# Performance work log

Measured on AMD Instinct MI355X. Metric: run time of the kernel, lower is better.

Reference implementation:

```python
import jax, jax.numpy as jnp
import numpy as np

NUM_S = 50000
NUM_A = 50000
D = 64
H = 128
E = 1000000


def setup_inputs() -> dict:
    key = jax.random.key(0)
    ks = jax.random.split(key, 6)
    scale = 1.0 / np.sqrt(2 * D)
    return {
        "embeddings_s": jax.random.normal(ks[0], (NUM_S, D), dtype=jnp.float32),
        "embeddings_a": jax.random.normal(ks[1], (NUM_A, D), dtype=jnp.float32),
        "edge_index_sa": jax.random.randint(ks[2], (2, E), 0, NUM_S, dtype=jnp.int64),
        "W1": jax.random.normal(ks[3], (2 * D, H), dtype=jnp.float32) * scale,
        "b1": jnp.zeros((H,), dtype=jnp.float32),
        "W2": jax.random.normal(ks[4], (H, 1), dtype=jnp.float32) * (1.0 / np.sqrt(H)),
        "b2": jnp.zeros((1,), dtype=jnp.float32),
        "log_temperature": jnp.zeros((), dtype=jnp.float32),  # log(1.0)
    }


def reference(embeddings_s, embeddings_a, edge_index_sa, W1, b1, W2, b2, log_temperature):
    s_idx = edge_index_sa[0]
    a_idx = edge_index_sa[1]
    es = embeddings_s[s_idx]            # [E, D] gather
    ea = embeddings_a[a_idx]            # [E, D] gather
    diff = es - ea
    edge_costs = jnp.sqrt(jnp.sum(diff * diff, axis=1))  # torch.norm(dim=1)
    cat = jnp.concatenate([es, ea], axis=1)              # [E, 2D]
    h = jax.nn.relu(cat @ W1 + b1)                        # [E, H]
    gate = jax.nn.sigmoid(h @ W2 + b2)[:, 0]             # [E]
    edge_costs = edge_costs * gate
    temperature = jnp.exp(log_temperature)
    vals = -edge_costs / temperature
    # scatter_softmax over edges grouped by source node
    seg_max = jax.ops.segment_max(vals, s_idx, num_segments=NUM_S)
    ex = jnp.exp(vals - seg_max[s_idx])
    seg_sum = jax.ops.segment_sum(ex, s_idx, num_segments=NUM_S)
    edge_weights = ex / seg_sum[s_idx]
    return (edge_weights, edge_costs)
```

## Files before the change

### kernel.cpp

```cpp
#include <hip/hip_runtime.h>
#include <hip/hip_fp16.h>

#define D_NODE 64
#define H_DIM  128
#define REC_H  192

struct Half8 { __half2 h[4]; };

typedef _Float16 h2v __attribute__((ext_vector_type(2)));
struct H2x4 { h2v h[4]; };

#if defined(__has_builtin)
#  if __has_builtin(__builtin_amdgcn_fdot2)
#    define HAVE_FDOT2 1
#  endif
#endif

__global__ void __launch_bounds__(256)
prep_kernel(const float* __restrict__ emb_s,
            const float* __restrict__ emb_a,
            const float* __restrict__ W1,
            const float* __restrict__ b1,
            __half* __restrict__ recS,
            __half* __restrict__ recA,
            float* __restrict__ segsum,
            int numS, int numA, int pS, int pA)
{
    const int tid = threadIdx.x;
    int b = blockIdx.x;

    if (b >= pS + pA) {
        const int i = (b - pS - pA) * 256 + tid;
        if (i < numS) segsum[i] = 0.0f;
        return;
    }

    const bool isS = (b < pS);
    const int pb = isS ? b : b - pS;
    const float* etab = isS ? emb_s : emb_a;
    __half* rec = isS ? recS : recA;
    const int rowsTot = isS ? numS : numA;
    const int rowBase = pb * 64;

    __shared__ __half eT[64 * D_NODE];

    {
        const float4* src4 = (const float4*)(etab + (size_t)rowBase * D_NODE);
#pragma unroll
        for (int it = 0; it < 2; ++it) {
            const int c = tid + it * 256;
            const int row = c >> 3;
            const int sub = c & 7;
            const bool ok = (rowBase + row < rowsTot);
            float4 a = make_float4(0.f, 0.f, 0.f, 0.f), d = a;
            if (ok) { a = src4[2 * c]; d = src4[2 * c + 1]; }
            Half8 o;
            o.h[0] = __floats2half2_rn(a.x, a.y);
            o.h[1] = __floats2half2_rn(a.z, a.w);
            o.h[2] = __floats2half2_rn(d.x, d.y);
            o.h[3] = __floats2half2_rn(d.z, d.w);
            ((Half8*)eT)[c] = o;
            if (ok)
                ((Half8*)(rec + (size_t)(rowBase + row) * REC_H))[sub] = o;
        }
    }

    const int col = tid & 127;
    const int rhalf = tid >> 7;
    const float* Wh = isS ? W1 : (W1 + D_NODE * H_DIM);
    h2v w2[32];
#pragma unroll
    for (int k = 0; k < 32; ++k) {
        w2[k][0] = (_Float16)Wh[(2 * k) * H_DIM + col];
        w2[k][1] = (_Float16)Wh[(2 * k + 1) * H_DIM + col];
    }
    const float bias = isS ? b1[col] : 0.0f;

    __syncthreads();

    for (int r0 = rhalf * 32; r0 < rhalf * 32 + 32; r0 += 4) {
        const H2x4* e0 = (const H2x4*)&eT[(r0 + 0) * D_NODE];
        const H2x4* e1 = (const H2x4*)&eT[(r0 + 1) * D_NODE];
        const H2x4* e2 = (const H2x4*)&eT[(r0 + 2) * D_NODE];
        const H2x4* e3 = (const H2x4*)&eT[(r0 + 3) * D_NODE];
        float a0 = bias, a1 = bias, a2 = bias, a3 = bias;
#pragma unroll
        for (int k8 = 0; k8 < D_NODE / 8; ++k8) {
            const H2x4 v0 = e0[k8];
            const H2x4 v1 = e1[k8];
            const H2x4 v2 = e2[k8];
            const H2x4 v3 = e3[k8];
#pragma unroll
            for (int j = 0; j < 4; ++j) {
                const h2v w = w2[4 * k8 + j];
#ifdef HAVE_FDOT2
                a0 = __builtin_amdgcn_fdot2(v0.h[j], w, a0, false);
                a1 = __builtin_amdgcn_fdot2(v1.h[j], w, a1, false);
                a2 = __builtin_amdgcn_fdot2(v2.h[j], w, a2, false);
                a3 = __builtin_amdgcn_fdot2(v3.h[j], w, a3, false);
#else
                const float wx = (float)w[0], wy = (float)w[1];
                a0 = fmaf((float)v0.h[j][0], wx, a0); a0 = fmaf((float)v0.h[j][1], wy, a0);
                a1 = fmaf((float)v1.h[j][0], wx, a1); a1 = fmaf((float)v1.h[j][1], wy, a1);
                a2 = fmaf((float)v2.h[j][0], wx, a2); a2 = fmaf((float)v2.h[j][1], wy, a2);
                a3 = fmaf((float)v3.h[j][0], wx, a3); a3 = fmaf((float)v3.h[j][1], wy, a3);
#endif
            }
        }
        const int row = rowBase + r0;
        if (row + 0 < rowsTot)
            rec[(size_t)(row + 0) * REC_H + D_NODE + col] = __float2half(a0);
        if (row + 1 < rowsTot)
            rec[(size_t)(row + 1) * REC_H + D_NODE + col] = __float2half(a1);
        if (row + 2 < rowsTot)
            rec[(size_t)(row + 2) * REC_H + D_NODE + col] = __float2half(a2);
        if (row + 3 < rowsTot)
            rec[(size_t)(row + 3) * REC_H + D_NODE + col] = __float2half(a3);
    }
}

__global__ void __launch_bounds__(256)
edge_main_kernel(const __half* __restrict__ recS,
                 const __half* __restrict__ recA,
                 const int* __restrict__ idx,
                 const float* __restrict__ W2,
                 const float* __restrict__ b2,
                 const float* __restrict__ logT,
                 float* __restrict__ out_costs,
                 float* __restrict__ segsum,
                 int E)
{
    const int gid = blockIdx.x * 256 + (int)threadIdx.x;
    const int p = gid >> 3;
    const int t = gid & 7;
    const int e0 = 2 * p;
    const int e1 = 2 * p + 1;
    if (e0 >= E) return;
    const bool has1 = (e1 < E);

    int s0, s1, a0, a1;
    {
        int2 sp = *(const int2*)(idx + e0);
        int2 ap = *(const int2*)(idx + E + e0);
        s0 = sp.x; s1 = has1 ? sp.y : sp.x;
        a0 = ap.x; a1 = has1 ? ap.y : ap.x;
    }

    const uint4* rs0 = (const uint4*)(recS + (size_t)s0 * REC_H);
    const uint4* ra0 = (const uint4*)(recA + (size_t)a0 * REC_H);
    const uint4* rs1 = (const uint4*)(recS + (size_t)s1 * REC_H);
    const uint4* ra1 = (const uint4*)(recA + (size_t)a1 * REC_H);

    uint4 es0 = rs0[t];
    uint4 ea0 = ra0[t];
    uint4 p0s_lo = rs0[8 + t];
    uint4 p0a_lo = ra0[8 + t];
    uint4 p0s_hi = rs0[16 + t];
    uint4 p0a_hi = ra0[16 + t];
    uint4 es1 = rs1[t];
    uint4 ea1 = ra1[t];
    uint4 p1s_lo = rs1[8 + t];
    uint4 p1a_lo = ra1[8 + t];
    uint4 p1s_hi = rs1[16 + t];
    uint4 p1a_hi = ra1[16 + t];

    const float4* w4 = (const float4*)W2;
    const float4 wl0 = w4[2 * t];
    const float4 wl1 = w4[2 * t + 1];
    const float4 wh0 = w4[2 * (t + 8)];
    const float4 wh1 = w4[2 * (t + 8) + 1];

    float n0 = 0.0f, g0 = 0.0f, n1 = 0.0f, g1 = 0.0f;

#define NORM_ACC(XS, XA, NACC)                                             \
    {                                                                      \
        const __half2* hs = (const __half2*)&XS;                           \
        const __half2* ha = (const __half2*)&XA;                           \
        _Pragma("unroll")                                                  \
        for (int k = 0; k < 4; ++k) {                                      \
            float2 fs = __half22float2(hs[k]);                             \
            float2 fa = __half22float2(ha[k]);                             \
            float d0 = fs.x - fa.x, d1 = fs.y - fa.y;                      \
            NACC = fmaf(d0, d0, NACC);                                     \
            NACC = fmaf(d1, d1, NACC);                                     \
        }                                                                  \
    }

#define GATE_ACC(PS, PA, W0, W1, G)                                        \
    {                                                                      \
        const __half2* hp = (const __half2*)&PS;                           \
        const __half2* hq = (const __half2*)&PA;                           \
        const float wv[8] = {W0.x, W0.y, W0.z, W0.w,                       \
                             W1.x, W1.y, W1.z, W1.w};                      \
        _Pragma("unroll")                                                  \
        for (int k = 0; k < 4; ++k) {                                      \
            float2 fp = __half22float2(hp[k]);                             \
            float2 fq = __half22float2(hq[k]);                             \
            float h0 = fmaxf(fp.x + fq.x, 0.0f);                           \
            float h1 = fmaxf(fp.y + fq.y, 0.0f);                           \
            G = fmaf(h0, wv[2 * k], G);                                    \
            G = fmaf(h1, wv[2 * k + 1], G);                                \
        }                                                                  \
    }

    NORM_ACC(es0, ea0, n0)
    GATE_ACC(p0s_lo, p0a_lo, wl0, wl1, g0)
    GATE_ACC(p0s_hi, p0a_hi, wh0, wh1, g0)
    NORM_ACC(es1, ea1, n1)
    GATE_ACC(p1s_lo, p1a_lo, wl0, wl1, g1)
    GATE_ACC(p1s_hi, p1a_hi, wh0, wh1, g1)

#pragma unroll
    for (int m = 1; m < 8; m <<= 1) {
        n0 += __shfl_xor(n0, m);
        g0 += __shfl_xor(g0, m);
        n1 += __shfl_xor(n1, m);
        g1 += __shfl_xor(g1, m);
    }

    if (t == 0) {
        const float temp = __expf(logT[0]);
        const float bb = b2[0];
        {
            const float gate = 1.0f / (1.0f + __expf(-(g0 + bb)));
            const float cost = sqrtf(n0) * gate;
            out_costs[e0] = cost;
            atomicAdd(&segsum[s0], __expf(-cost / temp));
        }
        if (has1) {
            const float gate = 1.0f / (1.0f + __expf(-(g1 + bb)));
            const float cost = sqrtf(n1) * gate;
            out_costs[e1] = cost;
            atomicAdd(&segsum[s1], __expf(-cost / temp));
        }
    }
#undef NORM_ACC
#undef GATE_ACC
}

__global__ void __launch_bounds__(256)
edge_norm_kernel(const int* __restrict__ idx,
                 const float* __restrict__ out_costs,
                 const float* __restrict__ segsum,
                 const float* __restrict__ logT,
                 float* __restrict__ out_w,
                 int E)
{
    const int e = blockIdx.x * blockDim.x + threadIdx.x;
    if (e >= E) return;
    const int s = idx[e];
    const float temp = __expf(logT[0]);
    const float ex = __expf(-out_costs[e] / temp);
    out_w[e] = ex / segsum[s];
}

extern "C" void kernel_launch(void* const* d_in, const int* in_sizes, int n_in,
                              void* d_out, int out_size, void* d_ws, size_t ws_size,
                              hipStream_t stream)
{
    const float* emb_s = (const float*)d_in[0];
    const float* emb_a = (const float*)d_in[1];
    const int*   idx   = (const int*)d_in[2];
    const float* W1    = (const float*)d_in[3];
    const float* b1    = (const float*)d_in[4];
    const float* W2    = (const float*)d_in[5];
    const float* b2    = (const float*)d_in[6];
    const float* logT  = (const float*)d_in[7];

    const int numS = in_sizes[0] / D_NODE;
    const int numA = in_sizes[1] / D_NODE;
    const int E    = in_sizes[2] / 2;

    float* out = (float*)d_out;

    char* ws = (char*)d_ws;
    __half* recS   = (__half*)ws;   ws += (size_t)numS * REC_H * sizeof(__half);
    __half* recA   = (__half*)ws;   ws += (size_t)numA * REC_H * sizeof(__half);
    float*  segsum = (float*)ws;

    const int pS = (numS + 63) / 64;
    const int pA = (numA + 63) / 64;
    const int zB = (numS + 255) / 256;
    prep_kernel<<<pS + pA + zB, 256, 0, stream>>>(emb_s, emb_a, W1, b1,
                                                  recS, recA, segsum,
                                                  numS, numA, pS, pA);

    {
        const int pairs = (E + 1) / 2;
        const long long threads = (long long)pairs * 8;
        const int blocks = (int)((threads + 255) / 256);
        edge_main_kernel<<<blocks, 256, 0, stream>>>(recS, recA, idx, W2, b2,
                                                     logT, out + E, segsum, E);
    }

    edge_norm_kernel<<<(E + 255) / 256, 256, 0, stream>>>(idx, out + E, segsum,
                                                          logT, out, E);
}
```

Before: 143.1 us.

## Bucket-sort edges by source node range before the edge gather kernel

Adds a histogram, scan and scatter pass that groups edges into buckets of source-node IDs, writing (s, a, edge id) records to a workspace array. The main edge kernel then reads edges in bucketed order, so the recS row gathers and segsum atomics are localized to a small range of source rows, which should improve cache hit rates. In exchange it adds three kernel launches, an extra 16 MB write and read of the sorted records, and global atomics on 512 cursors during the scatter. The recA gathers stay random, and costs are now written to scattered output positions.

```diff
diff --git a/kernel.cpp b/kernel.cpp
--- a/kernel.cpp
+++ b/kernel.cpp
@@ -4,6 +4,7 @@
 #define D_NODE 64
 #define H_DIM  128
 #define REC_H  192
+#define NBMAX  512
 
 struct Half8 { __half2 h[4]; };
 
@@ -24,6 +25,7 @@
             __half* __restrict__ recS,
             __half* __restrict__ recA,
             float* __restrict__ segsum,
+            unsigned* __restrict__ hist,
             int numS, int numA, int pS, int pA)
 {
     const int tid = threadIdx.x;
@@ -32,6 +34,7 @@
     if (b >= pS + pA) {
         const int i = (b - pS - pA) * 256 + tid;
         if (i < numS) segsum[i] = 0.0f;
+        if (i < NBMAX) hist[i] = 0u;
         return;
     }
 
@@ -120,9 +123,62 @@
 }
 
 __global__ void __launch_bounds__(256)
+hist_kernel(const int* __restrict__ idx,
+            unsigned* __restrict__ hist,
+            int E, int shift)
+{
+    __shared__ unsigned h[NBMAX];
+    const int tid = threadIdx.x;
+    for (int i = tid; i < NBMAX; i += 256) h[i] = 0u;
+    __syncthreads();
+
+    for (int e = blockIdx.x * 256 + tid; e < E; e += gridDim.x * 256)
+        atomicAdd(&h[(unsigned)idx[e] >> shift], 1u);
+
+    __syncthreads();
+    for (int i = tid; i < NBMAX; i += 256)
+        if (h[i]) atomicAdd(&hist[i], h[i]);
+}
+
+__global__ void __launch_bounds__(NBMAX)
+scan_kernel(const unsigned* __restrict__ hist,
+            unsigned* __restrict__ cursor)
+{
+    __shared__ unsigned buf[2][NBMAX];
+    const int tid = threadIdx.x;
+    const unsigned v = hist[tid];
+    buf[0][tid] = v;
+    __syncthreads();
+    int src = 0;
+#pragma unroll
+    for (int off = 1; off < NBMAX; off <<= 1) {
+        unsigned x = buf[src][tid];
+        if (tid >= off) x += buf[src][tid - off];
+        buf[src ^ 1][tid] = x;
+        src ^= 1;
+        __syncthreads();
+    }
+    cursor[tid] = buf[src][tid] - v;
+}
+
+__global__ void __launch_bounds__(256)
+scatter_kernel(const int* __restrict__ idx,
+               unsigned* __restrict__ cursor,
+               int4* __restrict__ sorted,
+               int E, int shift)
+{
+    const int e = blockIdx.x * 256 + (int)threadIdx.x;
+    if (e >= E) return;
+    const int s = idx[e];
+    const int a = idx[E + e];
+    const unsigned pos = atomicAdd(&cursor[(unsigned)s >> shift], 1u);
+    sorted[pos] = make_int4(s, a, e, 0);
+}
+
+__global__ void __launch_bounds__(256)
 edge_main_kernel(const __half* __restrict__ recS,
                  const __half* __restrict__ recA,
-                 const int* __restrict__ idx,
+                 const int4* __restrict__ sorted,
                  const float* __restrict__ W2,
                  const float* __restrict__ b2,
                  const float* __restrict__ logT,
@@ -138,13 +194,10 @@
     if (e0 >= E) return;
     const bool has1 = (e1 < E);
 
-    int s0, s1, a0, a1;
-    {
-        int2 sp = *(const int2*)(idx + e0);
-        int2 ap = *(const int2*)(idx + E + e0);
-        s0 = sp.x; s1 = has1 ? sp.y : sp.x;
-        a0 = ap.x; a1 = has1 ? ap.y : ap.x;
-    }
+    const int4 q0 = sorted[e0];
+    const int4 q1 = has1 ? sorted[e1] : q0;
+    const int s0 = q0.x, a0 = q0.y, oe0 = q0.z;
+    const int s1 = q1.x, a1 = q1.y, oe1 = q1.z;
 
     const uint4* rs0 = (const uint4*)(recS + (size_t)s0 * REC_H);
     const uint4* ra0 = (const uint4*)(recA + (size_t)a0 * REC_H);
@@ -224,13 +277,13 @@
         {
             const float gate = 1.0f / (1.0f + __expf(-(g0 + bb)));
             const float cost = sqrtf(n0) * gate;
-            out_costs[e0] = cost;
+            out_costs[oe0] = cost;
             atomicAdd(&segsum[s0], __expf(-cost / temp));
         }
         if (has1) {
             const float gate = 1.0f / (1.0f + __expf(-(g1 + bb)));
             const float cost = sqrtf(n1) * gate;
-            out_costs[e1] = cost;
+            out_costs[oe1] = cost;
             atomicAdd(&segsum[s1], __expf(-cost / temp));
         }
     }
@@ -273,23 +326,34 @@
 
     float* out = (float*)d_out;
 
+    int shift = 7;
+    while ((((numS - 1) >> shift) + 1) > NBMAX) ++shift;
+
     char* ws = (char*)d_ws;
-    __half* recS   = (__half*)ws;   ws += (size_t)numS * REC_H * sizeof(__half);
-    __half* recA   = (__half*)ws;   ws += (size_t)numA * REC_H * sizeof(__half);
-    float*  segsum = (float*)ws;
+    __half*   recS   = (__half*)ws;    ws += (size_t)numS * REC_H * sizeof(__half);
+    __half*   recA   = (__half*)ws;    ws += (size_t)numA * REC_H * sizeof(__half);
+    int4*     sorted = (int4*)ws;      ws += (size_t)E * sizeof(int4);
+    float*    segsum = (float*)ws;     ws += (size_t)numS * sizeof(float);
+    unsigned* hist   = (unsigned*)ws;  ws += NBMAX * sizeof(unsigned);
+    unsigned* cursor = (unsigned*)ws;
 
     const int pS = (numS + 63) / 64;
     const int pA = (numA + 63) / 64;
-    const int zB = (numS + 255) / 256;
+    const int zN = (numS > NBMAX ? numS : NBMAX);
+    const int zB = (zN + 255) / 256;
     prep_kernel<<<pS + pA + zB, 256, 0, stream>>>(emb_s, emb_a, W1, b1,
-                                                  recS, recA, segsum,
+                                                  recS, recA, segsum, hist,
                                                   numS, numA, pS, pA);
+
+    hist_kernel<<<512, 256, 0, stream>>>(idx, hist, E, shift);
+    scan_kernel<<<1, NBMAX, 0, stream>>>(hist, cursor);
+    scatter_kernel<<<(E + 255) / 256, 256, 0, stream>>>(idx, cursor, sorted, E, shift);
 
     {
         const int pairs = (E + 1) / 2;
         const long long threads = (long long)pairs * 8;
         const int blocks = (int)((threads + 255) / 256);
-        edge_main_kernel<<<blocks, 256, 0, stream>>>(recS, recA, idx, W2, b2,
+        edge_main_kernel<<<blocks, 256, 0, stream>>>(recS, recA, sorted, W2, b2,
                                                      logT, out + E, segsum, E);
     }
 
```

Result: slower. 501.8 us (+250.7%).
